# Kernel tuning notes

Measured on AMD Instinct MI355X. Metric: run time of the kernel, lower is better.

Reference implementation:

```python
import jax, jax.numpy as jnp
import numpy as np

B, S, D = 8, 2048, 512  # batch, seq_len, input_dim == qk_dim
K_SIZE = 6


def setup_inputs() -> dict:
    key = jax.random.key(0)
    ks = jax.random.split(key, 8)
    return {
        "evo_local": jax.random.normal(ks[0], (B, S, D), dtype=jnp.float32),
        "Wq": jax.random.normal(ks[1], (D, D), dtype=jnp.float32) * (1.0 / np.sqrt(D)),
        "bq": jax.random.normal(ks[2], (D,), dtype=jnp.float32) * 0.02,
        "dw_w": jax.random.normal(ks[3], (D, 1, K_SIZE), dtype=jnp.float32) * 0.1,  # depthwise conv (O, I/groups=1, K)
        "dw_b": jax.random.normal(ks[4], (D,), dtype=jnp.float32) * 0.02,
        "pw_w": jax.random.normal(ks[5], (D, D), dtype=jnp.float32) * (1.0 / np.sqrt(D)),  # pointwise 1x1 conv as matrix
        "pw_b": jax.random.normal(ks[6], (D,), dtype=jnp.float32) * 0.02,
        "pos": jax.random.normal(ks[7], (1, S, D), dtype=jnp.float32),
    }


def reference(evo_local, Wq, bq, dw_w, dw_b, pw_w, pw_b, pos):
    d = evo_local.shape[-1]
    # Q = Linear(evo_local) + learned positional encoding
    Q = jnp.einsum("bsd,ed->bse", evo_local, Wq) + bq + pos  # [B,S,D]

    # depthwise conv1d, kernel=6, torch padding='same' for even kernel -> pad (2, 3)
    x = jnp.transpose(evo_local, (0, 2, 1))  # [B,D,S]
    kv = jax.lax.conv_general_dilated(
        x, dw_w,
        window_strides=(1,),
        padding=[(2, 3)],
        feature_group_count=d,
        dimension_numbers=("NCH", "OIH", "NCH"),
    ) + dw_b[None, :, None]  # [B,D,S]
    # pointwise 1x1 conv
    kv = jnp.einsum("od,bds->bos", pw_w, kv) + pw_b[None, :, None]  # [B,D,S]
    KV = jnp.transpose(kv, (0, 2, 1))  # [B,S,D]; K and V share this

    scale = 1.0 / jnp.sqrt(jnp.float32(d))
    scores = jnp.einsum("bsd,btd->bst", Q, KV) * scale  # [B,S,S]
    attn = jax.nn.softmax(scores, axis=-1)
    out = jnp.einsum("bst,btd->bsd", attn, KV)
    return out + KV + evo_local
```

## Files before the change

### kernel.cpp

```cpp
#include <hip/hip_runtime.h>


typedef unsigned short ushort_t;
typedef __attribute__((ext_vector_type(8))) short short8;
typedef __attribute__((ext_vector_type(8))) unsigned short u16x8;
typedef __attribute__((ext_vector_type(4))) float f32x4;
typedef float4 f4;

__device__ __forceinline__ float bf2f(ushort_t h) {
    union { unsigned u; float f; } v; v.u = ((unsigned)h) << 16; return v.f;
}
__device__ __forceinline__ ushort_t f2bf(float f) {
    union { float f; unsigned u; } v; v.f = f;
    unsigned r = (v.u + 0x7FFFu + ((v.u >> 16) & 1u)) >> 16;
    return (ushort_t)r;
}

__device__ __forceinline__ void gld_lds16(const void* g, void* l) {
    __builtin_amdgcn_global_load_lds((const __attribute__((address_space(1))) void*)g,
                                     (__attribute__((address_space(3))) void*)l, 16, 0, 0);
}

template<int AF32, int EPI>
__global__ __launch_bounds__(256)
void mfma_nt(const void* __restrict__ Aptr, long long sA, int ldA,
             const ushort_t* __restrict__ Bh, long long sB, int ldB,
             int N, int K, float alpha,
             const float* __restrict__ bias, const float* __restrict__ pos,
             ushort_t* __restrict__ Ch, ushort_t* __restrict__ Cl, ushort_t* __restrict__ CTh,
             long long sC,
             float* __restrict__ Cf,
             const ushort_t* __restrict__ addH, const ushort_t* __restrict__ addL,
             const float* __restrict__ addF, long long sAdd)
{
    __shared__ __align__(16) ushort_t lds[8192];
    ushort_t* lAh = lds;
    ushort_t* lBh = lds + 4096;

    const int t = threadIdx.x;
    const int w = t >> 6, lane = t & 63;
    const int z = blockIdx.z;
    const ushort_t* Ab = (const ushort_t*)Aptr + (long long)z * sA;
    const float*    Af = (const float*)Aptr    + (long long)z * sA;
    Bh += (long long)z * sB;

    const int m0 = blockIdx.y * 128, n0 = blockIdx.x * 128;
    const int wr = w >> 1, wc = w & 1;
    const int fr = lane & 15, kg = lane >> 4;
    const int srow = lane >> 2;
    const int scol = (lane & 3) * 8;

    const f32x4 zero = {0.f, 0.f, 0.f, 0.f};
    f32x4 acc[4][4];
#pragma unroll
    for (int i = 0; i < 4; ++i)
#pragma unroll
        for (int j = 0; j < 4; ++j) acc[i][j] = zero;

    for (int k0 = 0; k0 < K; k0 += 32) {
#pragma unroll
        for (int i = 0; i < 2; ++i) {
            const int g = w * 2 + i;
            const int row = g * 16 + srow;
            if (AF32) {
                const float* p = Af + (long long)(m0 + row) * ldA + k0 + scol;
                f4 v0 = *(const f4*)p;
                f4 v1 = *(const f4*)(p + 4);
                u16x8 o;
                o[0] = f2bf(v0.x); o[1] = f2bf(v0.y); o[2] = f2bf(v0.z); o[3] = f2bf(v0.w);
                o[4] = f2bf(v1.x); o[5] = f2bf(v1.y); o[6] = f2bf(v1.z); o[7] = f2bf(v1.w);
                *(u16x8*)&lAh[g * 512 + srow * 32 + scol] = o;
            } else {
                gld_lds16(Ab + (long long)(m0 + row) * ldA + k0 + scol, &lAh[g * 512]);
            }
            gld_lds16(Bh + (long long)(n0 + row) * ldB + k0 + scol, &lBh[g * 512]);
        }
        __syncthreads();

        short8 aH[4];
#pragma unroll
        for (int fm = 0; fm < 4; ++fm)
            aH[fm] = *(const short8*)&lAh[(wr * 64 + fm * 16 + fr) * 32 + kg * 8];
#pragma unroll
        for (int fn = 0; fn < 4; ++fn) {
            short8 bH = *(const short8*)&lBh[(wc * 64 + fn * 16 + fr) * 32 + kg * 8];
#pragma unroll
            for (int fm = 0; fm < 4; ++fm)
                acc[fm][fn] = __builtin_amdgcn_mfma_f32_16x16x32_bf16(aH[fm], bH, acc[fm][fn], 0, 0, 0);
        }
        __syncthreads();
    }

#pragma unroll
    for (int fm = 0; fm < 4; ++fm)
#pragma unroll
    for (int fn = 0; fn < 4; ++fn)
#pragma unroll
    for (int r = 0; r < 4; ++r) {
        const int m = m0 + wr * 64 + fm * 16 + kg * 4 + r;
        const int n = n0 + wc * 64 + fn * 16 + fr;
        float v = acc[fm][fn][r];
        const long long idx = (long long)m * N + n;
        if (EPI == 0) {
            v += bias[n] + pos[(long long)(m & 2047) * N + n];
            Ch[idx] = f2bf(v);
        } else if (EPI == 1) {
            v += bias[n];
            ushort_t hi = f2bf(v);
            Ch[idx] = hi;
            Cl[idx] = f2bf(v - bf2f(hi));
            CTh[(long long)(m >> 11) * (512LL * 2048) + (long long)n * 2048 + (m & 2047)] = hi;
        } else if (EPI == 2) {
            Ch[(long long)z * sC + idx] = f2bf(v * alpha);
        } else {
            const long long o = (long long)z * sAdd + idx;
            v += bf2f(addH[o]) + bf2f(addL[o]) + addF[o];
            Cf[o] = v;
        }
    }
}

__global__ __launch_bounds__(256)
void cvt2_bf16(const float* __restrict__ a, ushort_t* __restrict__ ao,
               const float* __restrict__ b, ushort_t* __restrict__ bo)
{
    int i = blockIdx.x * 256 + threadIdx.x;
    const float* src = (i < 65536) ? a : b;
    ushort_t* dst = (i < 65536) ? ao : bo;
    int j = i & 65535;
    f4 v = *(const f4*)(src + (long long)j * 4);
    ushort4 o;
    o.x = f2bf(v.x); o.y = f2bf(v.y); o.z = f2bf(v.z); o.w = f2bf(v.w);
    *(ushort4*)&dst[(long long)j * 4] = o;
}

__global__ __launch_bounds__(256)
void dwconv_bf16(const float* __restrict__ x, const float* __restrict__ w,
                 const float* __restrict__ bias, ushort_t* __restrict__ y)
{
    const int tid = blockIdx.x * 256 + threadIdx.x;
    const int d4 = tid & 127;
    const int rest = tid >> 7;
    const int sc = rest & 255;
    const int b = rest >> 8;
    const int s0 = sc * 8;
    const float* xb = x + ((long long)b * 2048) * 512 + d4 * 4;

    f4 win[13];
#pragma unroll
    for (int j = 0; j < 13; ++j) {
        int r = s0 + j - 2;
        int rc = r < 0 ? 0 : (r > 2047 ? 2047 : r);
        f4 v = *(const f4*)(xb + (long long)rc * 512);
        if (r < 0 || r > 2047) { v.x = 0.f; v.y = 0.f; v.z = 0.f; v.w = 0.f; }
        win[j] = v;
    }
    float wk[4][6];
#pragma unroll
    for (int dd = 0; dd < 4; ++dd)
#pragma unroll
        for (int k = 0; k < 6; ++k) wk[dd][k] = w[(d4 * 4 + dd) * 6 + k];
    const f4 bs4 = *(const f4*)(bias + d4 * 4);

    ushort_t* yb = y + ((long long)b * 2048 + s0) * 512 + d4 * 4;
#pragma unroll
    for (int u = 0; u < 8; ++u) {
        float a0 = bs4.x, a1 = bs4.y, a2 = bs4.z, a3 = bs4.w;
#pragma unroll
        for (int k = 0; k < 6; ++k) {
            f4 v = win[u + k];
            a0 = fmaf(v.x, wk[0][k], a0);
            a1 = fmaf(v.y, wk[1][k], a1);
            a2 = fmaf(v.z, wk[2][k], a2);
            a3 = fmaf(v.w, wk[3][k], a3);
        }
        ushort4 o;
        o.x = f2bf(a0); o.y = f2bf(a1); o.z = f2bf(a2); o.w = f2bf(a3);
        *(ushort4*)(yb + (long long)u * 512) = o;
    }
}

__global__ __launch_bounds__(256)
void softmax_bf16(ushort_t* __restrict__ p)
{
    ushort_t* row = p + ((long long)blockIdx.x << 11);
    const int t = threadIdx.x;
    __shared__ float redMax[4];
    __shared__ float redSum[4];

    u16x8 u = *(const u16x8*)(row + t * 8);
    float x[8];
#pragma unroll
    for (int i = 0; i < 8; ++i) x[i] = bf2f(u[i]);

    float m = x[0];
#pragma unroll
    for (int i = 1; i < 8; ++i) m = fmaxf(m, x[i]);
#pragma unroll
    for (int off = 32; off > 0; off >>= 1) m = fmaxf(m, __shfl_xor(m, off));
    if ((t & 63) == 0) redMax[t >> 6] = m;
    __syncthreads();
    m = fmaxf(fmaxf(redMax[0], redMax[1]), fmaxf(redMax[2], redMax[3]));

    float e[8], s = 0.f;
#pragma unroll
    for (int i = 0; i < 8; ++i) { e[i] = __expf(x[i] - m); s += e[i]; }
#pragma unroll
    for (int off = 32; off > 0; off >>= 1) s += __shfl_xor(s, off);
    if ((t & 63) == 0) redSum[t >> 6] = s;
    __syncthreads();
    s = (redSum[0] + redSum[1]) + (redSum[2] + redSum[3]);
    const float inv = 1.0f / s;

#pragma unroll
    for (int i = 0; i < 8; ++i) u[i] = f2bf(e[i] * inv);
    *(u16x8*)(row + t * 8) = u;
}

extern "C" void kernel_launch(void* const* d_in, const int* in_sizes, int n_in,
                              void* d_out, int out_size, void* d_ws, size_t ws_size,
                              hipStream_t stream)
{
    const float* evo  = (const float*)d_in[0];
    const float* Wq   = (const float*)d_in[1];
    const float* bq   = (const float*)d_in[2];
    const float* dw_w = (const float*)d_in[3];
    const float* dw_b = (const float*)d_in[4];
    const float* pw_w = (const float*)d_in[5];
    const float* pw_b = (const float*)d_in[6];
    const float* pos  = (const float*)d_in[7];
    float* out = (float*)d_out;

    const long long BSD = 8LL * 2048 * 512;
    const long long DD  = 512LL * 512;
    const long long SD  = 2048LL * 512;
    const long long SS  = 2048LL * 2048;

    ushort_t* QHi  = (ushort_t*)d_ws;
    ushort_t* KVHi = QHi + BSD;
    ushort_t* KVLo = KVHi + BSD;
    ushort_t* KVT  = KVLo + BSD;
    ushort_t* WqB  = KVT + BSD;
    ushort_t* pwB  = WqB + DD;
    ushort_t* X    = pwB + DD;

    long long Xbytes = (long long)ws_size - 68157440LL;
    long long cRaw = Xbytes / (SS * 2);
    int c;
    if (cRaw >= 8) c = 8; else if (cRaw >= 4) c = 4; else if (cRaw >= 2) c = 2; else c = 1;

    ushort_t* dwout = X;

    cvt2_bf16<<<512, 256, 0, stream>>>(Wq, WqB, pw_w, pwB);

    dwconv_bf16<<<1024, 256, 0, stream>>>(evo, dw_w, dw_b, dwout);

    mfma_nt<1, 0><<<dim3(4, 128, 1), 256, 0, stream>>>(
        evo, 0LL, 512, WqB, 0LL, 512, 512, 512, 1.f,
        bq, pos, QHi, nullptr, nullptr, 0LL, nullptr, nullptr, nullptr, nullptr, 0LL);

    mfma_nt<0, 1><<<dim3(4, 128, 1), 256, 0, stream>>>(
        dwout, 0LL, 512, pwB, 0LL, 512, 512, 512, 1.f,
        pw_b, nullptr, KVHi, KVLo, KVT, 0LL, nullptr, nullptr, nullptr, nullptr, 0LL);

    const float scale = 0.04419417382415922f;
    for (int b0 = 0; b0 < 8; b0 += c) {
        const int cc = (8 - b0 < c) ? (8 - b0) : c;
        const long long o = (long long)b0 * SD;
        mfma_nt<0, 2><<<dim3(16, 16, cc), 256, 0, stream>>>(
            QHi + o, SD, 512, KVHi + o, SD, 512, 2048, 512, scale,
            nullptr, nullptr, X, nullptr, nullptr, SS, nullptr, nullptr, nullptr, nullptr, 0LL);
        softmax_bf16<<<cc * 2048, 256, 0, stream>>>(X);
        mfma_nt<0, 3><<<dim3(4, 16, cc), 256, 0, stream>>>(
            X, SS, 2048, KVT + o, SD, 2048, 512, 2048, 1.f,
            nullptr, nullptr, nullptr, nullptr, nullptr, 0LL,
            out + o, KVHi + o, KVLo + o, evo + o, SD);
    }
}
```

Before: 304.7 us.

## Add 256x256-tile pipelined MFMA GEMM for attention score and PV products

Result: no change. 304.2 us (-0.2%).

```diff
diff --git a/kernel.cpp b/kernel.cpp
--- a/kernel.cpp
+++ b/kernel.cpp
@@ -19,6 +19,136 @@
 __device__ __forceinline__ void gld_lds16(const void* g, void* l) {
     __builtin_amdgcn_global_load_lds((const __attribute__((address_space(1))) void*)g,
                                      (__attribute__((address_space(3))) void*)l, 16, 0, 0);
+}
+
+#define BAR()   asm volatile("s_barrier" ::: "memory")
+#define WAITV8  do { asm volatile("s_waitcnt vmcnt(8)" ::: "memory"); __builtin_amdgcn_sched_barrier(0); } while (0)
+#define WAITV0  do { asm volatile("s_waitcnt vmcnt(0)" ::: "memory"); __builtin_amdgcn_sched_barrier(0); } while (0)
+#define WAITL   do { asm volatile("s_waitcnt lgkmcnt(0)" ::: "memory"); __builtin_amdgcn_sched_barrier(0); } while (0)
+
+template<int EPI>
+__global__ __launch_bounds__(512, 2)
+void mfma_nt256(const ushort_t* __restrict__ A, long long sA, int ldA,
+                const ushort_t* __restrict__ B, long long sB, int ldB,
+                int N, int K, float alpha,
+                ushort_t* __restrict__ Ch, long long sC,
+                float* __restrict__ Cf,
+                const ushort_t* __restrict__ addH, const ushort_t* __restrict__ addL,
+                const float* __restrict__ addF, long long sAdd)
+{
+    __shared__ __align__(16) ushort_t lds[65536];
+
+    const int t = threadIdx.x;
+    const int w = t >> 6, lane = t & 63;
+    const int z = blockIdx.z;
+    A += (long long)z * sA;
+    B += (long long)z * sB;
+    const int m0 = blockIdx.y * 256, n0 = blockIdx.x * 256;
+    const int wr = w >> 2, wc = w & 3;
+    const int fr = lane & 15, kg = lane >> 4;
+    const int nkt = K >> 6;
+
+    const int sRo = lane >> 2;
+    const long long sCk = ((lane & 3) ^ ((lane >> 3) & 3)) * 8;
+    const int co = (kg ^ ((fr >> 1) & 3)) * 8;
+
+#define STAGE(P, base0, ld, segbase, h, Ts) do {                                         \
+    const long long kk_ = (long long)(((Ts) < nkt ? (Ts) : (nkt - 1)) * 64 + (h) * 32) + sCk; \
+    const int g0_ = w * 2;                                                               \
+    gld_lds16((P) + (long long)((base0) + g0_ * 16 + sRo) * (ld) + kk_,                  \
+              &lds[(segbase) + g0_ * 512]);                                              \
+    gld_lds16((P) + (long long)((base0) + g0_ * 16 + 16 + sRo) * (ld) + kk_,             \
+              &lds[(segbase) + g0_ * 512 + 512]);                                        \
+} while (0)
+
+#define AREAD(ksseg) do {                                                                \
+    const int ab_ = (ksseg) * 8192 + wr * 4096 + fr * 32 + co;                           \
+    _Pragma("unroll") for (int fm_ = 0; fm_ < 8; ++fm_)                                  \
+        afr[fm_] = *(const short8*)&lds[ab_ + fm_ * 512];                                \
+} while (0)
+
+#define BREAD(ksseg, fnh) do {                                                           \
+    const int bb_ = 32768 + (ksseg) * 8192 + wc * 2048 + (fnh) * 1024 + fr * 32 + co;    \
+    bfr[0] = *(const short8*)&lds[bb_];                                                  \
+    bfr[1] = *(const short8*)&lds[bb_ + 512];                                            \
+} while (0)
+
+#define MF2(j0) do {                                                                     \
+    __builtin_amdgcn_s_setprio(1);                                                       \
+    _Pragma("unroll") for (int fm_ = 0; fm_ < 8; ++fm_) {                                \
+        acc[fm_][(j0)]     = __builtin_amdgcn_mfma_f32_16x16x32_bf16(afr[fm_], bfr[0], acc[fm_][(j0)], 0, 0, 0);     \
+        acc[fm_][(j0) + 1] = __builtin_amdgcn_mfma_f32_16x16x32_bf16(afr[fm_], bfr[1], acc[fm_][(j0) + 1], 0, 0, 0); \
+    }                                                                                    \
+    __builtin_amdgcn_s_setprio(0);                                                       \
+} while (0)
+
+    const f32x4 zero = {0.f, 0.f, 0.f, 0.f};
+    f32x4 acc[8][4];
+#pragma unroll
+    for (int i = 0; i < 8; ++i)
+#pragma unroll
+        for (int j = 0; j < 4; ++j) acc[i][j] = zero;
+
+    short8 afr[8], bfr[2];
+
+    STAGE(A, m0, ldA, 0,             0, 0);
+    STAGE(B, n0, ldB, 32768,         0, 0);
+    STAGE(A, m0, ldA, 8192,          1, 0);
+    STAGE(B, n0, ldB, 32768 + 8192,  1, 0);
+    STAGE(A, m0, ldA, 16384,         0, 1);
+    STAGE(B, n0, ldB, 32768 + 16384, 0, 1);
+    WAITV8;
+    BAR();
+
+    for (int kt = 0; kt < nkt; ++kt) {
+        const int b = kt & 1, nb = b ^ 1;
+        AREAD(b * 2); BREAD(b * 2, 0);
+        STAGE(A, m0, ldA, (nb * 2 + 1) * 8192, 1, kt + 1);
+        BAR(); WAITL;
+        MF2(0);
+        BAR();
+        BREAD(b * 2, 1);
+        STAGE(B, n0, ldB, 32768 + (nb * 2 + 1) * 8192, 1, kt + 1);
+        BAR(); WAITL;
+        MF2(2);
+        WAITV8;
+        BAR();
+        AREAD(b * 2 + 1); BREAD(b * 2 + 1, 0);
+        STAGE(A, m0, ldA, (b * 2) * 8192, 0, kt + 2);
+        BAR(); WAITL;
+        MF2(0);
+        BAR();
+        BREAD(b * 2 + 1, 1);
+        STAGE(B, n0, ldB, 32768 + (b * 2) * 8192, 0, kt + 2);
+        BAR(); WAITL;
+        MF2(2);
+        WAITV8;
+        BAR();
+    }
+    WAITV0;
+
+#pragma unroll
+    for (int fm = 0; fm < 8; ++fm)
+#pragma unroll
+    for (int fn = 0; fn < 4; ++fn)
+#pragma unroll
+    for (int r = 0; r < 4; ++r) {
+        const int m = m0 + wr * 128 + fm * 16 + kg * 4 + r;
+        const int n = n0 + wc * 64 + fn * 16 + fr;
+        float v = acc[fm][fn][r];
+        const long long idx = (long long)m * N + n;
+        if (EPI == 2) {
+            Ch[(long long)z * sC + idx] = f2bf(v * alpha);
+        } else {
+            const long long o = (long long)z * sAdd + idx;
+            v += bf2f(addH[o]) + bf2f(addL[o]) + addF[o];
+            Cf[o] = v;
+        }
+    }
+#undef STAGE
+#undef AREAD
+#undef BREAD
+#undef MF2
 }
 
 template<int AF32, int EPI>
@@ -28,10 +158,7 @@
              int N, int K, float alpha,
              const float* __restrict__ bias, const float* __restrict__ pos,
              ushort_t* __restrict__ Ch, ushort_t* __restrict__ Cl, ushort_t* __restrict__ CTh,
-             long long sC,
-             float* __restrict__ Cf,
-             const ushort_t* __restrict__ addH, const ushort_t* __restrict__ addL,
-             const float* __restrict__ addF, long long sAdd)
+             long long sC)
 {
     __shared__ __align__(16) ushort_t lds[8192];
     ushort_t* lAh = lds;
@@ -104,18 +231,12 @@
         if (EPI == 0) {
             v += bias[n] + pos[(long long)(m & 2047) * N + n];
             Ch[idx] = f2bf(v);
-        } else if (EPI == 1) {
+        } else {
             v += bias[n];
             ushort_t hi = f2bf(v);
             Ch[idx] = hi;
             Cl[idx] = f2bf(v - bf2f(hi));
             CTh[(long long)(m >> 11) * (512LL * 2048) + (long long)n * 2048 + (m & 2047)] = hi;
-        } else if (EPI == 2) {
-            Ch[(long long)z * sC + idx] = f2bf(v * alpha);
-        } else {
-            const long long o = (long long)z * sAdd + idx;
-            v += bf2f(addH[o]) + bf2f(addL[o]) + addF[o];
-            Cf[o] = v;
         }
     }
 }
@@ -252,28 +373,26 @@
     ushort_t* dwout = X;
 
     cvt2_bf16<<<512, 256, 0, stream>>>(Wq, WqB, pw_w, pwB);
-
     dwconv_bf16<<<1024, 256, 0, stream>>>(evo, dw_w, dw_b, dwout);
 
     mfma_nt<1, 0><<<dim3(4, 128, 1), 256, 0, stream>>>(
         evo, 0LL, 512, WqB, 0LL, 512, 512, 512, 1.f,
-        bq, pos, QHi, nullptr, nullptr, 0LL, nullptr, nullptr, nullptr, nullptr, 0LL);
+        bq, pos, QHi, nullptr, nullptr, 0LL);
 
     mfma_nt<0, 1><<<dim3(4, 128, 1), 256, 0, stream>>>(
         dwout, 0LL, 512, pwB, 0LL, 512, 512, 512, 1.f,
-        pw_b, nullptr, KVHi, KVLo, KVT, 0LL, nullptr, nullptr, nullptr, nullptr, 0LL);
+        pw_b, nullptr, KVHi, KVLo, KVT, 0LL);
 
     const float scale = 0.04419417382415922f;
     for (int b0 = 0; b0 < 8; b0 += c) {
         const int cc = (8 - b0 < c) ? (8 - b0) : c;
         const long long o = (long long)b0 * SD;
-        mfma_nt<0, 2><<<dim3(16, 16, cc), 256, 0, stream>>>(
+        mfma_nt256<2><<<dim3(8, 8, cc), 512, 0, stream>>>(
             QHi + o, SD, 512, KVHi + o, SD, 512, 2048, 512, scale,
-            nullptr, nullptr, X, nullptr, nullptr, SS, nullptr, nullptr, nullptr, nullptr, 0LL);
+            X, SS, nullptr, nullptr, nullptr, nullptr, 0LL);
         softmax_bf16<<<cc * 2048, 256, 0, stream>>>(X);
-        mfma_nt<0, 3><<<dim3(4, 16, cc), 256, 0, stream>>>(
+        mfma_nt256<3><<<dim3(2, 8, cc), 512, 0, stream>>>(
             X, SS, 2048, KVT + o, SD, 2048, 512, 2048, 1.f,
-            nullptr, nullptr, nullptr, nullptr, nullptr, 0LL,
-            out + o, KVHi + o, KVLo + o, evo + o, SD);
-    }
-}
+            nullptr, 0LL, out + o, KVHi + o, KVLo + o, evo + o, SD);
+    }
+}
```
